# Kernel tuning notes

Measured on AMD Instinct MI355X. Metric: run time of the kernel, lower is better.

The kernel has to match this reference:

```python
import jax, jax.numpy as jnp
import numpy as np
from jax import lax


def conv2d(x, w, b, pad):
    # x: NCHW, w: OIHW
    out = lax.conv_general_dilated(x, w, (1, 1), [(pad, pad), (pad, pad)],
                                   dimension_numbers=('NCHW', 'OIHW', 'NCHW'))
    return out + b[None, :, None, None]


def traj_grid_sample(ps, gx, gy):
    """Faithful F.grid_sample (5D, trilinear, zeros padding, align_corners=False)
    applied to ps expanded along a depth axis of size L. Since every depth slice
    of the expanded input equals ps, we gather 2D from ps and fold the z-axis
    interpolation weights / bounds mask in analytically (no (B,C,L,H,W) expand).
    ps: (B,C,H,W); gx, gy: (B,L,H,W) pixel-coordinate flow fields."""
    B, C, H, W = ps.shape
    L = gx.shape[1]
    dt = ps.dtype
    # the original normalizes to [-1,1] assuming align_corners-style ranges
    gxn = gx / (W - 1) * 2 - 1
    gyn = gy / (H - 1) * 2 - 1
    gzn = jnp.arange(1, L + 1, dtype=dt) / (L - 1) * 2 - 1  # (L,)
    # torch grid_sample default align_corners=False unnormalization
    ix = ((gxn + 1) * W - 1) / 2
    iy = ((gyn + 1) * H - 1) / 2
    iz = jnp.broadcast_to((((gzn + 1) * L - 1) / 2)[None, :, None, None], ix.shape)
    x0 = jnp.floor(ix)
    y0 = jnp.floor(iy)
    z0 = jnp.floor(iz)
    bidx = jnp.arange(B)[:, None, None, None]
    out = jnp.zeros((B, L, H, W, C), dtype=dt)
    for dz in (0.0, 1.0):
        zc = z0 + dz
        wz = 1.0 - jnp.abs(iz - zc)
        mz = (zc >= 0) & (zc <= L - 1)
        for dy in (0.0, 1.0):
            yc = y0 + dy
            wy = 1.0 - jnp.abs(iy - yc)
            my = (yc >= 0) & (yc <= H - 1)
            yci = jnp.clip(yc, 0, H - 1).astype(jnp.int32)
            for dx in (0.0, 1.0):
                xc = x0 + dx
                wx = 1.0 - jnp.abs(ix - xc)
                mx = (xc >= 0) & (xc <= W - 1)
                xci = jnp.clip(xc, 0, W - 1).astype(jnp.int32)
                w = wz * wy * wx * (mz & my & mx).astype(dt)  # (B,L,H,W)
                val = ps[bidx, :, yci, xci]  # (B,L,H,W,C)
                out = out + val * w[..., None]
    return jnp.transpose(out, (0, 4, 1, 2, 3))  # (B,C,L,H,W)


def reference(x, prev_state, sub_w1, sub_b1, sub_w2, sub_b2,
              reset_w, reset_b, update_w, update_b, out_w, out_b,
              reset_ww, reset_wb, update_ww, update_wb, out_ww, out_wb):
    B, Ch, H, W = prev_state.shape
    L = sub_w2.shape[0] // 2
    # subCNN: flow generation
    s = jnp.concatenate([x, prev_state], axis=1)
    o = jax.nn.relu(conv2d(s, sub_w1, sub_b1, 2))
    o = jax.nn.relu(conv2d(o, sub_w2, sub_b2, 2))
    M = traj_grid_sample(prev_state, o[:, :L], o[:, L:])  # (B,Ch,L,H,W)
    Mf = M.reshape(B, Ch * L, H, W)  # view(B, C*L, H, W)
    update = jax.nn.sigmoid(conv2d(x, update_w, update_b, 1) + conv2d(Mf, update_ww, update_wb, 0))
    reset = jax.nn.sigmoid(conv2d(x, reset_w, reset_b, 1) + conv2d(Mf, reset_ww, reset_wb, 0))
    v = conv2d(x, out_w, out_b, 1) + reset * conv2d(Mf, out_ww, out_wb, 0)
    out_inputs = jnp.where(v >= 0, v, 0.2 * v)  # leaky_relu(0.2)
    return prev_state * update + out_inputs * (1.0 - update)


def setup_inputs() -> dict:
    key = jax.random.key(0)
    ks = jax.random.split(key, 12)
    B, Cin, Ch, L, H, W = 4, 8, 96, 13, 96, 96
    rn = lambda k, shape, s=0.05: jax.random.normal(k, shape, dtype=jnp.float32) * s
    z = lambda n: jnp.zeros((n,), jnp.float32)
    return {
        'x': rn(ks[0], (B, Cin, H, W), 1.0),
        'prev_state': rn(ks[1], (B, Ch, H, W), 1.0),
        'sub_w1': rn(ks[2], (32, Cin + Ch, 5, 5)), 'sub_b1': z(32),
        'sub_w2': rn(ks[3], (2 * L, 32, 5, 5)), 'sub_b2': z(2 * L),
        'reset_w': rn(ks[4], (Ch, Cin, 3, 3)), 'reset_b': z(Ch),
        'update_w': rn(ks[5], (Ch, Cin, 3, 3)), 'update_b': z(Ch),
        'out_w': rn(ks[6], (Ch, Cin, 3, 3)), 'out_b': z(Ch),
        'reset_ww': rn(ks[7], (Ch, Ch * L, 1, 1)), 'reset_wb': z(Ch),
        'update_ww': rn(ks[8], (Ch, Ch * L, 1, 1)), 'update_wb': z(Ch),
        'out_ww': rn(ks[9], (Ch, Ch * L, 1, 1)), 'out_wb': z(Ch),
    }
```

## Files before the change

kernel.cpp:

```cpp
#include <hip/hip_runtime.h>
#include <hip/hip_bf16.h>

#define HW 9216

typedef unsigned short ushort;
typedef unsigned int   uint;
typedef __attribute__((ext_vector_type(4))) float f32x4;
typedef __attribute__((ext_vector_type(2))) uint  u32x2;
typedef __attribute__((ext_vector_type(4))) uint  u32x4;
typedef __attribute__((ext_vector_type(4))) int   i32x4;
typedef __attribute__((ext_vector_type(8))) short s16x8;

__device__ float  g_o1[4*32*HW];
__device__ float  g_q [2*4*26*HW];
__device__ __align__(16) float g_ht[4*HW*96];
__device__ __align__(16) ushort g_chi[4*(size_t)HW*128];
__device__ __align__(16) ushort g_clo[4*(size_t)HW*128];
__device__ __align__(16) ushort g_w1b[28*4*2048];
__device__ __align__(16) ushort g_b[18*39*512];
__device__ __align__(16) float  g_urv[2304*288*16];

__device__ __forceinline__ ushort f2b(float f){
  uint x = __float_as_uint(f);
  return (ushort)((x + 0x7FFFu + ((x >> 16) & 1u)) >> 16);
}
__device__ __forceinline__ float b2f(ushort h){
  return __uint_as_float(((uint)h) << 16);
}

__global__ void pack_b_k(const float* __restrict__ uww, const float* __restrict__ rww,
                         const float* __restrict__ vww){
  int i = blockIdx.x*256 + threadIdx.x;
  if (i >= 3*96*1248) return;
  int gate = i / (96*1248); int rem = i % (96*1248);
  int oc = rem / 1248;      int kp = rem % 1248;
  int l = kp / 96, c = kp % 96;
  const float* src = (gate == 0) ? uww : ((gate == 1) ? rww : vww);
  float v = src[oc*1248 + c*13 + l];
  int n  = gate*96 + oc;
  int nt = n >> 4, nl = n & 15;
  int kb = kp >> 5, kk = kp & 31;
  g_b[(nt*39 + kb)*512 + ((kk >> 3)*16 + nl)*8 + (kk & 7)] = f2b(v);
}

__global__ void pack_w1b_k(const float* __restrict__ w1){
  int i = blockIdx.x*256 + threadIdx.x;
  if (i >= 25*4*1024) return;
  int tap = i >> 12;
  int cb  = (i >> 10) & 3;
  int oc  = (i >> 5) & 31;
  int kk  = i & 31;
  int ci  = cb*32 + kk;
  float w = (ci < 104) ? w1[oc*2600 + ci*25 + tap] : 0.f;
  ushort h = f2b(w);
  float rem = w - b2f(h);
  int base = ((tap*4 + cb) << 11) + (oc >> 4)*512 + (oc & 15)*32 + kk;
  g_w1b[base]        = h;
  g_w1b[base + 1024] = f2b(rem);
}

__global__ __launch_bounds__(256) void transpose_k(const float* __restrict__ hp,
                                                   const float* __restrict__ x){
  __shared__ float tile[32][33];
  int s0 = blockIdx.x*32;
  int b  = blockIdx.z;
  int t  = threadIdx.x;
  if (blockIdx.y < 3){
    int c0 = blockIdx.y*32;
    for (int i = t; i < 32*32; i += 256){
      int c = i >> 5, s = i & 31;
      tile[c][s] = hp[((size_t)(b*96 + c0 + c))*HW + s0 + s];
    }
    __syncthreads();
    for (int i = t; i < 32*32; i += 256){
      int s = i >> 5, c = i & 31;
      float v = tile[c][s];
      size_t px = (size_t)b*HW + s0 + s;
      g_ht[px*96 + c0 + c] = v;
      ushort h = f2b(v);
      g_chi[px*128 + 8 + c0 + c] = h;
      g_clo[px*128 + 8 + c0 + c] = f2b(v - b2f(h));
    }
  } else {
    for (int i = t; i < 8*32; i += 256){
      int c = i >> 5, s = i & 31;
      tile[c][s] = x[((size_t)(b*8 + c))*HW + s0 + s];
    }
    __syncthreads();
    for (int i = t; i < 32*8; i += 256){
      int s = i >> 3, c = i & 7;
      float v = tile[c][s];
      size_t px = (size_t)b*HW + s0 + s;
      ushort h = f2b(v);
      g_chi[px*128 + c] = h;
      g_clo[px*128 + c] = f2b(v - b2f(h));
    }
  }
}

__global__ __launch_bounds__(256) void conv1_mfma_k(const float* __restrict__ b1){
  __shared__ __align__(16) ushort sh[2*160*128];
  int t = threadIdx.x;
  int w = t >> 6, lane = t & 63;
  int nl = lane & 15, q = lane >> 4;
  int rt = blockIdx.x / 6, ct = blockIdx.x % 6;
  int b  = blockIdx.z;
  int r0 = rt*4, c0 = ct*16;
  const size_t pbase = (size_t)b*HW;

  #pragma unroll
  for (int i = 0; i < 20; i++){
    int idx = i*256 + t;
    int half = (i >= 10) ? 1 : 0;
    int rem = idx - half*2560;
    int px = rem >> 4, ci = rem & 15;
    int cs = ci ^ (px & 15);
    int r = px / 20, c = px - r*20;
    int gr = r0 + r - 2, gc = c0 + c - 2;
    f32x4 v = (f32x4){0.f,0.f,0.f,0.f};
    if ((unsigned)gr < 96u && (unsigned)gc < 96u){
      const ushort* src = half ? g_clo : g_chi;
      v = *(const f32x4*)(src + ((pbase + (size_t)(gr*96 + gc)) << 7) + cs*8);
    }
    *(f32x4*)((char*)sh + (size_t)idx*16) = v;
  }
  __syncthreads();

  int kxA[7], kyA[7], tpA[7];
  #pragma unroll
  for (int i = 0; i < 7; i++){
    int tp  = 7*w + i;
    int tpc = (tp > 24) ? 24 : tp;
    kyA[i] = tpc / 5;
    kxA[i] = tpc - kyA[i]*5;
    tpA[i] = tp;
  }
  int foff = nl*32 + q*8;

  f32x4 acc[4][2];
  #pragma unroll
  for (int mr = 0; mr < 4; mr++){
    acc[mr][0] = (f32x4){0.f,0.f,0.f,0.f};
    acc[mr][1] = (f32x4){0.f,0.f,0.f,0.f};
  }

  for (int cb = 0; cb < 4; cb++){
    const ushort* bpc = g_w1b + ((size_t)cb << 11);
    s16x8 bq[3][4];
#define LOADB(slot, i) { const ushort* bp = bpc + ((size_t)tpA[i] << 13); \
    bq[slot][0] = *(const s16x8*)(bp + foff); \
    bq[slot][1] = *(const s16x8*)(bp + 512 + foff); \
    bq[slot][2] = *(const s16x8*)(bp + 1024 + foff); \
    bq[slot][3] = *(const s16x8*)(bp + 1536 + foff); }
    LOADB(0, 0); LOADB(1, 1);

    #pragma unroll
    for (int i = 0; i < 7; i++){
      if (i < 5) LOADB((i + 2) % 3, i + 2);
      int ky = kyA[i], kx = kxA[i];
      int chq = cb*4 + q;
      s16x8 ah[4], al[4];
      #pragma unroll
      for (int mr = 0; mr < 4; mr++){
        int px  = (mr + ky)*20 + kx + nl;
        int off = px*256 + (((chq ^ (px & 15))) << 4);
        ah[mr] = *(const s16x8*)((const char*)sh + off);
        al[mr] = *(const s16x8*)((const char*)sh + 40960 + off);
      }
      const int cur = i % 3;
      #pragma unroll
      for (int mr = 0; mr < 4; mr++){
        acc[mr][0] = __builtin_amdgcn_mfma_f32_16x16x32_bf16(ah[mr], bq[cur][0], acc[mr][0], 0,0,0);
        acc[mr][1] = __builtin_amdgcn_mfma_f32_16x16x32_bf16(ah[mr], bq[cur][1], acc[mr][1], 0,0,0);
      }
      #pragma unroll
      for (int mr = 0; mr < 4; mr++){
        acc[mr][0] = __builtin_amdgcn_mfma_f32_16x16x32_bf16(al[mr], bq[cur][0], acc[mr][0], 0,0,0);
        acc[mr][1] = __builtin_amdgcn_mfma_f32_16x16x32_bf16(al[mr], bq[cur][1], acc[mr][1], 0,0,0);
      }
      #pragma unroll
      for (int mr = 0; mr < 4; mr++){
        acc[mr][0] = __builtin_amdgcn_mfma_f32_16x16x32_bf16(ah[mr], bq[cur][2], acc[mr][0], 0,0,0);
        acc[mr][1] = __builtin_amdgcn_mfma_f32_16x16x32_bf16(ah[mr], bq[cur][3], acc[mr][1], 0,0,0);
      }
    }
#undef LOADB
  }

  __syncthreads();
  float* red = (float*)sh;
  #pragma unroll
  for (int mr = 0; mr < 4; mr++)
    #pragma unroll
    for (int nt = 0; nt < 2; nt++)
      *(f32x4*)&red[(((mr*2 + nt)*4 + w) << 8) + lane*4] = acc[mr][nt];
  __syncthreads();

  int mr = w;
  #pragma unroll
  for (int nt = 0; nt < 2; nt++){
    f32x4 s = (f32x4){0.f,0.f,0.f,0.f};
    #pragma unroll
    for (int ww = 0; ww < 4; ww++)
      s += *(f32x4*)&red[(((mr*2 + nt)*4 + ww) << 8) + lane*4];
    int oc = nt*16 + nl;
    float bias = b1[oc];
    s.x = fmaxf(s.x + bias, 0.f); s.y = fmaxf(s.y + bias, 0.f);
    s.z = fmaxf(s.z + bias, 0.f); s.w = fmaxf(s.w + bias, 0.f);
    *(f32x4*)(g_o1 + ((size_t)(b*32 + oc))*HW + (size_t)(r0 + mr)*96 + c0 + q*4) = s;
  }
}

__global__ __launch_bounds__(256) void conv2_k(const float* __restrict__ wt2,
                                               const float* __restrict__ b2){
  __shared__ __align__(16) float in_sh[8][20][24];
  __shared__ __align__(16) float w_sh[8][25][32];
  int tile = blockIdx.x;
  int kg   = blockIdx.y;
  int b    = blockIdx.z;
  int row0 = (tile / 6) * 16, col0 = (tile % 6) * 16;
  int t = threadIdx.x;
  int og  = t >> 5;
  int pos = t & 31;
  int row = pos >> 1, x0 = (pos & 1)*8;

  float acc[8][4];
  #pragma unroll
  for (int j = 0; j < 8; j++)
    #pragma unroll
    for (int o = 0; o < 4; o++) acc[j][o] = 0.f;

  for (int cc = 0; cc < 2; cc++){
    __syncthreads();
    for (int idx = t; idx < 8*20*24; idx += 256){
      int i = idx / 480, rem = idx % 480;
      int r = rem / 24, c = rem % 24;
      int gr = row0 + r - 2, gc = col0 + c - 2;
      float v = 0.f;
      if ((unsigned)gr < 96u && (unsigned)gc < 96u){
        int ci = kg*16 + cc*8 + i;
        v = g_o1[(b*32 + ci)*HW + gr*96 + gc];
      }
      in_sh[i][r][c] = v;
    }
    for (int idx = t; idx < 8*25*32; idx += 256){
      int i = idx / 800, rem = idx % 800;
      int tap = rem / 32, oc = rem % 32;
      int ci = kg*16 + cc*8 + i;
      w_sh[i][tap][oc] = (oc < 26) ? wt2[oc*800 + ci*25 + tap] : 0.f;
    }
    __syncthreads();

    for (int i = 0; i < 8; i++){
      #pragma unroll
      for (int ky = 0; ky < 5; ky++){
        const float* rp = &in_sh[i][row + ky][x0];
        f32x4 s0 = *(const f32x4*)(rp);
        f32x4 s1 = *(const f32x4*)(rp + 4);
        f32x4 s2 = *(const f32x4*)(rp + 8);
        float seg[12] = {s0.x,s0.y,s0.z,s0.w, s1.x,s1.y,s1.z,s1.w, s2.x,s2.y,s2.z,s2.w};
        #pragma unroll
        for (int kx = 0; kx < 5; kx++){
          f32x4 wv = *(const f32x4*)&w_sh[i][ky*5 + kx][og*4];
          #pragma unroll
          for (int j = 0; j < 8; j++){
            float a = seg[kx + j];
            acc[j][0] += a*wv.x; acc[j][1] += a*wv.y;
            acc[j][2] += a*wv.z; acc[j][3] += a*wv.w;
          }
        }
      }
    }
  }

  int rg = row0 + row, cg = col0 + x0;
  #pragma unroll
  for (int o = 0; o < 4; o++){
    int slot = og*4 + o;
    if (slot < 26){
      float bias = (kg == 0) ? b2[slot] : 0.f;
      float* d = g_q + (size_t)kg*4*26*HW + ((size_t)(b*26 + slot))*HW + rg*96 + cg;
      #pragma unroll
      for (int j = 0; j < 8; j++) d[j] = acc[j][o] + bias;
    }
  }
}

__global__ __launch_bounds__(256) void gemm_k(){
  __shared__ __align__(16) ushort Bsh[18*512];
  __shared__ __align__(16) float cw4[13][64][4];
  __shared__ __align__(16) int   co4[13][64][4];
  int t = threadIdx.x;
  int w = t >> 6, lane = t & 63;
  int nl = lane & 15, quad = lane >> 4;
  int blk = blockIdx.x;
  int b   = blk / 144;
  int pbase0 = (blk % 144) * 64;
  int pt  = blk*4 + w;

  const int NQ = 4*26*HW;
  for (int idx = t; idx < 832; idx += 256){
    int l = idx >> 6, m = idx & 63;
    int p = pbase0 + m;
    float gx = fmaxf(g_q[(b*26 + l     )*HW + p] + g_q[NQ + (b*26 + l     )*HW + p], 0.f);
    float gy = fmaxf(g_q[(b*26 + 13 + l)*HW + p] + g_q[NQ + (b*26 + 13 + l)*HW + p], 0.f);
    float ix = gx * (96.f/95.f) - 0.5f;
    float iy = gy * (96.f/95.f) - 0.5f;
    float iz = (float)(l+1) * (13.f/12.f) - 0.5f;
    float z0 = floorf(iz);
    float zf = 0.f;
    #pragma unroll
    for (int dz = 0; dz < 2; dz++){
      float zc = z0 + (float)dz;
      float wz = 1.f - fabsf(iz - zc);
      if (zc >= 0.f && zc <= 12.f) zf += wz;
    }
    float x0f = floorf(ix), y0f = floorf(iy);
    #pragma unroll
    for (int dy = 0; dy < 2; dy++){
      float yc = y0f + (float)dy;
      float wy = 1.f - fabsf(iy - yc);
      bool  my = (yc >= 0.f) && (yc <= 95.f);
      int  yci = min(max((int)yc, 0), 95);
      #pragma unroll
      for (int dx = 0; dx < 2; dx++){
        float xc = x0f + (float)dx;
        float wx = 1.f - fabsf(ix - xc);
        bool  mx = (xc >= 0.f) && (xc <= 95.f);
        int  xci = min(max((int)xc, 0), 95);
        cw4[l][m][dy*2+dx] = (mx && my) ? zf*wy*wx : 0.f;
        co4[l][m][dy*2+dx] = yci*96 + xci;
      }
    }
  }

  f32x4 acc[18];
  #pragma unroll
  for (int nt = 0; nt < 18; nt++) acc[nt] = (f32x4){0.f,0.f,0.f,0.f};

  const u32x2* Bg8 = reinterpret_cast<const u32x2*>(g_b);
  const float* hb = g_ht + (size_t)b*HW*96 + quad*8;
  int mloc = w*16 + nl;

  f32x4 gA[8], gB[8], wA, wB;
  u32x2 sA[9], sB[9];

  #pragma unroll
  for (int u = 0; u < 9; u++){
    int idx8 = u*256 + t;
    sA[u] = Bg8[((idx8 >> 7)*39 + 0)*128 + (idx8 & 127)];
  }
  __syncthreads();

  {
    wA = *(const f32x4*)cw4[0][mloc];
    i32x4 ov_ = *(const i32x4*)co4[0][mloc];
    const float* q0_ = hb + (size_t)ov_.x*96;
    const float* q1_ = hb + (size_t)ov_.y*96;
    const float* q2_ = hb + (size_t)ov_.z*96;
    const float* q3_ = hb + (size_t)ov_.w*96;
    gA[0]=*(const f32x4*)q0_; gA[1]=*(const f32x4*)(q0_+4);
    gA[2]=*(const f32x4*)q1_; gA[3]=*(const f32x4*)(q1_+4);
    gA[4]=*(const f32x4*)q2_; gA[5]=*(const f32x4*)(q2_+4);
    gA[6]=*(const f32x4*)q3_; gA[7]=*(const f32x4*)(q3_+4);
  }
  int ln = 0, k3n = 1;

#define BODY(KB, GC, WC, GN, WN, SC, SN, PF) { \
  if (PF){ \
    _Pragma("unroll") \
    for (int u = 0; u < 9; u++){ \
      int idx8 = u*256 + t; \
      SN[u] = Bg8[((idx8 >> 7)*39 + (KB) + 1)*128 + (idx8 & 127)]; \
    } \
    WN = *(const f32x4*)cw4[ln][mloc]; \
    i32x4 ov_ = *(const i32x4*)co4[ln][mloc]; \
    const float* hc_ = hb + k3n*32; \
    const float* q0_ = hc_ + (size_t)ov_.x*96; \
    const float* q1_ = hc_ + (size_t)ov_.y*96; \
    const float* q2_ = hc_ + (size_t)ov_.z*96; \
    const float* q3_ = hc_ + (size_t)ov_.w*96; \
    GN[0]=*(const f32x4*)q0_; GN[1]=*(const f32x4*)(q0_+4); \
    GN[2]=*(const f32x4*)q1_; GN[3]=*(const f32x4*)(q1_+4); \
    GN[4]=*(const f32x4*)q2_; GN[5]=*(const f32x4*)(q2_+4); \
    GN[6]=*(const f32x4*)q3_; GN[7]=*(const f32x4*)(q3_+4); \
    k3n++; if (k3n == 3){ k3n = 0; ln++; } \
  } \
  _Pragma("unroll") \
  for (int u = 0; u < 9; u++){ \
    int idx8 = u*256 + t; \
    *(u32x2*)((char*)Bsh + idx8*8) = SC[u]; \
  } \
  f32x4 aA = WC.x*GC[0] + WC.y*GC[2] + WC.z*GC[4] + WC.w*GC[6]; \
  f32x4 aB = WC.x*GC[1] + WC.y*GC[3] + WC.z*GC[5] + WC.w*GC[7]; \
  union { u32x4 u4; s16x8 s8v; } cv_; \
  cv_.u4.x = (uint)f2b(aA.x) | ((uint)f2b(aA.y) << 16); \
  cv_.u4.y = (uint)f2b(aA.z) | ((uint)f2b(aA.w) << 16); \
  cv_.u4.z = (uint)f2b(aB.x) | ((uint)f2b(aB.y) << 16); \
  cv_.u4.w = (uint)f2b(aB.z) | ((uint)f2b(aB.w) << 16); \
  asm volatile("s_waitcnt lgkmcnt(0)" ::: "memory"); \
  __builtin_amdgcn_s_barrier(); \
  asm volatile("" ::: "memory"); \
  _Pragma("unroll") \
  for (int nt = 0; nt < 18; nt++){ \
    s16x8 bf = *(const s16x8*)((const char*)Bsh + nt*1024 + lane*16); \
    acc[nt] = __builtin_amdgcn_mfma_f32_16x16x32_bf16(cv_.s8v, bf, acc[nt], 0, 0, 0); \
  } \
  asm volatile("" ::: "memory"); \
  __builtin_amdgcn_s_barrier(); \
  asm volatile("" ::: "memory"); \
}

  for (int kb = 0; kb < 38; kb += 2){
    BODY(kb,     gA, wA, gB, wB, sA, sB, 1);
    BODY(kb + 1, gB, wB, gA, wA, sB, sA, 1);
  }
  BODY(38, gA, wA, gB, wB, sA, sB, 0);
#undef BODY

  float* dst = g_urv + (size_t)pt*4608;
  #pragma unroll
  for (int nt = 0; nt < 18; nt++)
    *(f32x4*)&dst[(nt*16 + nl)*16 + quad*4] = acc[nt];
}

__global__ __launch_bounds__(256) void gate_k(const float* __restrict__ x,
                        const float* __restrict__ hp,
                        const float* __restrict__ uw, const float* __restrict__ ub,
                        const float* __restrict__ rw, const float* __restrict__ rb,
                        const float* __restrict__ vw, const float* __restrict__ vb,
                        const float* __restrict__ uwb, const float* __restrict__ rwb,
                        const float* __restrict__ vwb, float* __restrict__ out){
  int p  = blockIdx.x*256 + threadIdx.x;
  int oc = blockIdx.y;
  int b  = blockIdx.z;
  int h = p/96, w = p%96;
  float xU = ub[oc], xR = rb[oc], xV = vb[oc];
  const float* xb = x + b*8*HW;
  for (int ky = 0; ky < 3; ky++){
    int r = h+ky-1;
    if ((unsigned)r >= 96u) continue;
    for (int kx = 0; kx < 3; kx++){
      int c = w+kx-1;
      if ((unsigned)c >= 96u) continue;
      int off = r*96 + c;
      int wo  = ky*3 + kx;
      #pragma unroll
      for (int ic = 0; ic < 8; ic++){
        float a = xb[ic*HW + off];
        xU += a * uw[oc*72 + ic*9 + wo];
        xR += a * rw[oc*72 + ic*9 + wo];
        xV += a * vw[oc*72 + ic*9 + wo];
      }
    }
  }
  int pt = b*576 + (p >> 4), px = p & 15;
  const float* ur = g_urv + (size_t)pt*4608 + px;
  float gU = ur[(0*96 + oc)*16] + uwb[oc];
  float gR = ur[(1*96 + oc)*16] + rwb[oc];
  float gV = ur[(2*96 + oc)*16] + vwb[oc];
  float u = 1.f / (1.f + __expf(-(xU + gU)));
  float r = 1.f / (1.f + __expf(-(xR + gR)));
  float v = xV + r * gV;
  float oi = (v >= 0.f) ? v : 0.2f*v;
  float h0 = hp[(b*96 + oc)*HW + p];
  out[(b*96 + oc)*HW + p] = h0*u + oi*(1.f - u);
}

extern "C" void kernel_launch(void* const* d_in, const int* in_sizes, int n_in,
                              void* d_out, int out_size, void* d_ws, size_t ws_size,
                              hipStream_t stream){
  const float* x    = (const float*)d_in[0];
  const float* hp   = (const float*)d_in[1];
  const float* sw1  = (const float*)d_in[2];
  const float* sb1  = (const float*)d_in[3];
  const float* sw2  = (const float*)d_in[4];
  const float* sb2  = (const float*)d_in[5];
  const float* rw   = (const float*)d_in[6];
  const float* rb   = (const float*)d_in[7];
  const float* uw   = (const float*)d_in[8];
  const float* ub   = (const float*)d_in[9];
  const float* vw   = (const float*)d_in[10];
  const float* vb   = (const float*)d_in[11];
  const float* rww  = (const float*)d_in[12];
  const float* rwb  = (const float*)d_in[13];
  const float* uww  = (const float*)d_in[14];
  const float* uwb  = (const float*)d_in[15];
  const float* vww  = (const float*)d_in[16];
  const float* vwb  = (const float*)d_in[17];

  pack_b_k    <<<dim3((3*96*1248 + 255)/256), dim3(256), 0, stream>>>(uww, rww, vww);
  pack_w1b_k  <<<dim3((25*4*1024 + 255)/256), dim3(256), 0, stream>>>(sw1);
  transpose_k <<<dim3(288, 4, 4), dim3(256), 0, stream>>>(hp, x);
  conv1_mfma_k<<<dim3(144, 1, 4), dim3(256), 0, stream>>>(sb1);
  conv2_k     <<<dim3(36, 2, 4), dim3(256), 0, stream>>>(sw2, sb2);
  gemm_k      <<<dim3(576),      dim3(256), 0, stream>>>();
  gate_k      <<<dim3(36, 96, 4), dim3(256), 0, stream>>>(x, hp,
               uw, ub, rw, rb, vw, vb, uwb, rwb, vwb, (float*)d_out);
}
```

Baseline: 380.8 us.

## Store hidden-state gather table in fp16 and skip zero-weight depth slice

The transposed hidden-state buffer used by the trajectory gather is now stored as fp16 instead of fp32, so each corner fetch is one 16-byte load instead of two. This halves the bytes pulled by the random gathers in gemm_k. The GEMM K loop also drops the last depth slice (l=12), whose trilinear z weights are always zero, going from 39 to 36 K-blocks. fp16 storage adds rounding before the bf16 conversion, which could slightly change numerical error.

```diff
diff --git a/kernel.cpp b/kernel.cpp
--- a/kernel.cpp
+++ b/kernel.cpp
@@ -10,10 +10,11 @@
 typedef __attribute__((ext_vector_type(4))) uint  u32x4;
 typedef __attribute__((ext_vector_type(4))) int   i32x4;
 typedef __attribute__((ext_vector_type(8))) short s16x8;
+typedef __attribute__((ext_vector_type(8))) _Float16 f16x8;
 
 __device__ float  g_o1[4*32*HW];
 __device__ float  g_q [2*4*26*HW];
-__device__ __align__(16) float g_ht[4*HW*96];
+__device__ __align__(16) _Float16 g_hh[4*(size_t)HW*96];
 __device__ __align__(16) ushort g_chi[4*(size_t)HW*128];
 __device__ __align__(16) ushort g_clo[4*(size_t)HW*128];
 __device__ __align__(16) ushort g_w1b[28*4*2048];
@@ -76,7 +77,7 @@
       int s = i >> 5, c = i & 31;
       float v = tile[c][s];
       size_t px = (size_t)b*HW + s0 + s;
-      g_ht[px*96 + c0 + c] = v;
+      g_hh[px*96 + c0 + c] = (_Float16)v;
       ushort h = f2b(v);
       g_chi[px*128 + 8 + c0 + c] = h;
       g_clo[px*128 + 8 + c0 + c] = f2b(v - b2f(h));
@@ -288,8 +289,8 @@
 
 __global__ __launch_bounds__(256) void gemm_k(){
   __shared__ __align__(16) ushort Bsh[18*512];
-  __shared__ __align__(16) float cw4[13][64][4];
-  __shared__ __align__(16) int   co4[13][64][4];
+  __shared__ __align__(16) float cw4[12][64][4];
+  __shared__ __align__(16) int   co4[12][64][4];
   int t = threadIdx.x;
   int w = t >> 6, lane = t & 63;
   int nl = lane & 15, quad = lane >> 4;
@@ -299,7 +300,7 @@
   int pt  = blk*4 + w;
 
   const int NQ = 4*26*HW;
-  for (int idx = t; idx < 832; idx += 256){
+  for (int idx = t; idx < 768; idx += 256){
     int l = idx >> 6, m = idx & 63;
     int p = pbase0 + m;
     float gx = fmaxf(g_q[(b*26 + l     )*HW + p] + g_q[NQ + (b*26 + l     )*HW + p], 0.f);
@@ -339,10 +340,11 @@
   for (int nt = 0; nt < 18; nt++) acc[nt] = (f32x4){0.f,0.f,0.f,0.f};
 
   const u32x2* Bg8 = reinterpret_cast<const u32x2*>(g_b);
-  const float* hb = g_ht + (size_t)b*HW*96 + quad*8;
+  const _Float16* hb = g_hh + (size_t)b*HW*96 + quad*8;
   int mloc = w*16 + nl;
 
-  f32x4 gA[8], gB[8], wA, wB;
+  f16x8 gA[4], gB[4];
+  f32x4 wA, wB;
   u32x2 sA[9], sB[9];
 
   #pragma unroll
@@ -355,14 +357,10 @@
   {
     wA = *(const f32x4*)cw4[0][mloc];
     i32x4 ov_ = *(const i32x4*)co4[0][mloc];
-    const float* q0_ = hb + (size_t)ov_.x*96;
-    const float* q1_ = hb + (size_t)ov_.y*96;
-    const float* q2_ = hb + (size_t)ov_.z*96;
-    const float* q3_ = hb + (size_t)ov_.w*96;
-    gA[0]=*(const f32x4*)q0_; gA[1]=*(const f32x4*)(q0_+4);
-    gA[2]=*(const f32x4*)q1_; gA[3]=*(const f32x4*)(q1_+4);
-    gA[4]=*(const f32x4*)q2_; gA[5]=*(const f32x4*)(q2_+4);
-    gA[6]=*(const f32x4*)q3_; gA[7]=*(const f32x4*)(q3_+4);
+    gA[0] = *(const f16x8*)(hb + (size_t)ov_.x*96);
+    gA[1] = *(const f16x8*)(hb + (size_t)ov_.y*96);
+    gA[2] = *(const f16x8*)(hb + (size_t)ov_.z*96);
+    gA[3] = *(const f16x8*)(hb + (size_t)ov_.w*96);
   }
   int ln = 0, k3n = 1;
 
@@ -375,15 +373,11 @@
     } \
     WN = *(const f32x4*)cw4[ln][mloc]; \
     i32x4 ov_ = *(const i32x4*)co4[ln][mloc]; \
-    const float* hc_ = hb + k3n*32; \
-    const float* q0_ = hc_ + (size_t)ov_.x*96; \
-    const float* q1_ = hc_ + (size_t)ov_.y*96; \
-    const float* q2_ = hc_ + (size_t)ov_.z*96; \
-    const float* q3_ = hc_ + (size_t)ov_.w*96; \
-    GN[0]=*(const f32x4*)q0_; GN[1]=*(const f32x4*)(q0_+4); \
-    GN[2]=*(const f32x4*)q1_; GN[3]=*(const f32x4*)(q1_+4); \
-    GN[4]=*(const f32x4*)q2_; GN[5]=*(const f32x4*)(q2_+4); \
-    GN[6]=*(const f32x4*)q3_; GN[7]=*(const f32x4*)(q3_+4); \
+    const _Float16* hc_ = hb + k3n*32; \
+    GN[0] = *(const f16x8*)(hc_ + (size_t)ov_.x*96); \
+    GN[1] = *(const f16x8*)(hc_ + (size_t)ov_.y*96); \
+    GN[2] = *(const f16x8*)(hc_ + (size_t)ov_.z*96); \
+    GN[3] = *(const f16x8*)(hc_ + (size_t)ov_.w*96); \
     k3n++; if (k3n == 3){ k3n = 0; ln++; } \
   } \
   _Pragma("unroll") \
@@ -391,13 +385,16 @@
     int idx8 = u*256 + t; \
     *(u32x2*)((char*)Bsh + idx8*8) = SC[u]; \
   } \
-  f32x4 aA = WC.x*GC[0] + WC.y*GC[2] + WC.z*GC[4] + WC.w*GC[6]; \
-  f32x4 aB = WC.x*GC[1] + WC.y*GC[3] + WC.z*GC[5] + WC.w*GC[7]; \
+  float av[8]; \
+  _Pragma("unroll") \
+  for (int j = 0; j < 8; j++) \
+    av[j] = WC.x*(float)GC[0][j] + WC.y*(float)GC[1][j] \
+          + WC.z*(float)GC[2][j] + WC.w*(float)GC[3][j]; \
   union { u32x4 u4; s16x8 s8v; } cv_; \
-  cv_.u4.x = (uint)f2b(aA.x) | ((uint)f2b(aA.y) << 16); \
-  cv_.u4.y = (uint)f2b(aA.z) | ((uint)f2b(aA.w) << 16); \
-  cv_.u4.z = (uint)f2b(aB.x) | ((uint)f2b(aB.y) << 16); \
-  cv_.u4.w = (uint)f2b(aB.z) | ((uint)f2b(aB.w) << 16); \
+  cv_.u4.x = (uint)f2b(av[0]) | ((uint)f2b(av[1]) << 16); \
+  cv_.u4.y = (uint)f2b(av[2]) | ((uint)f2b(av[3]) << 16); \
+  cv_.u4.z = (uint)f2b(av[4]) | ((uint)f2b(av[5]) << 16); \
+  cv_.u4.w = (uint)f2b(av[6]) | ((uint)f2b(av[7]) << 16); \
   asm volatile("s_waitcnt lgkmcnt(0)" ::: "memory"); \
   __builtin_amdgcn_s_barrier(); \
   asm volatile("" ::: "memory"); \
@@ -411,11 +408,12 @@
   asm volatile("" ::: "memory"); \
 }
 
-  for (int kb = 0; kb < 38; kb += 2){
+  for (int kb = 0; kb < 34; kb += 2){
     BODY(kb,     gA, wA, gB, wB, sA, sB, 1);
     BODY(kb + 1, gB, wB, gA, wA, sB, sA, 1);
   }
-  BODY(38, gA, wA, gB, wB, sA, sB, 0);
+  BODY(34, gA, wA, gB, wB, sA, sB, 1);
+  BODY(35, gB, wB, gA, wA, sB, sA, 0);
 #undef BODY
 
   float* dst = g_urv + (size_t)pt*4608;
```

After: 346.0 us. -9.1%, faster.
